# Kernel tuning notes

Measured on AMD Instinct MI355X. Metric: run time of the kernel, lower is better.

Reference implementation:

```python
import jax, jax.numpy as jnp
import numpy as np

D_MODEL = 1024
STATE_DIM = 256
BATCH = 4
SEQ_LEN = 4096


def setup_inputs() -> dict:
    key = jax.random.key(0)
    k_u, k_B, k_C = jax.random.split(key, 3)
    u = jax.random.normal(k_u, (BATCH, SEQ_LEN, D_MODEL), dtype=jnp.float32)
    # parameters (as in torch init)
    log_lambda = jnp.linspace(2.94, 4.6, STATE_DIM, dtype=jnp.float32)
    # nn.Linear weight shape is [out_features, in_features]
    B_w = jax.random.normal(k_B, (STATE_DIM, D_MODEL), dtype=jnp.float32) / np.sqrt(D_MODEL)
    C_w = jax.random.normal(k_C, (D_MODEL, STATE_DIM), dtype=jnp.float32) / np.sqrt(STATE_DIM)
    D = jnp.ones((D_MODEL,), dtype=jnp.float32)
    return {"u": u, "log_lambda": log_lambda, "B_w": B_w, "C_w": C_w, "D": D}


def reference(u, log_lambda, B_w, C_w, D):
    batch, seq_len, d = u.shape
    # Bu = B(u): [B, L, N]
    Bu = jnp.einsum("bld,nd->bln", u, B_w)
    lam = jax.nn.sigmoid(log_lambda)                     # [N]
    t = jnp.arange(seq_len, dtype=lam.dtype)
    kernel = lam[None, :] ** t[:, None]                  # [L, N]
    # next power of two >= 2*L (static)
    fft_len = 1
    while fft_len < 2 * seq_len:
        fft_len *= 2
    K_hat = jnp.fft.rfft(kernel, n=fft_len, axis=0)      # [F, N]
    Bu_hat = jnp.fft.rfft(Bu, n=fft_len, axis=1)         # [B, F, N]
    h_hat = K_hat[None, :, :] * Bu_hat
    h = jnp.fft.irfft(h_hat, n=fft_len, axis=1)[:, :seq_len, :]  # [B, L, N]
    y = jnp.einsum("bln,dn->bld", h, C_w) + D * u
    return y
```

## Files before the change

### kernel.cpp

```cpp
#include <hip/hip_runtime.h>
#include <hip/hip_bf16.h>

#define D_MODEL 1024
#define STATE_N 256
#define BATCH 4
#define SEQ_LEN 4096
#define M_TOTAL (BATCH * SEQ_LEN)
#define NCHUNK 128
#define CHUNK (SEQ_LEN / NCHUNK)

typedef __attribute__((ext_vector_type(8))) short bf16x8;
typedef __attribute__((ext_vector_type(4))) short s16x4;
typedef __attribute__((ext_vector_type(2))) short s16x2;
typedef __attribute__((ext_vector_type(4))) float f32x4;

static __device__ inline short f2bf(float f) {
    union { float f; unsigned u; } v; v.f = f;
    unsigned r = v.u + 0x7FFFu + ((v.u >> 16) & 1u);
    return (short)(r >> 16);
}
static __device__ inline float bf2f(short s) {
    union { unsigned u; float f; } v;
    v.u = ((unsigned)(unsigned short)s) << 16;
    return v.f;
}
static __device__ inline float sigmoidf(float x) { return 1.0f / (1.0f + expf(-x)); }

#define GLOAD_LDS16(gp, lp)                                                     \
    __builtin_amdgcn_global_load_lds(                                           \
        (const __attribute__((address_space(1))) void*)(gp),                    \
        (__attribute__((address_space(3))) void*)(lp), 16, 0, 0)

#define WAITVM0   asm volatile("s_waitcnt vmcnt(0)" ::: "memory")
#define WAITLGKM0 asm volatile("s_waitcnt lgkmcnt(0)" ::: "memory")
#define BARRIER() do { __builtin_amdgcn_s_barrier(); asm volatile("" ::: "memory"); } while (0)

__global__ void prep(const float* __restrict__ Bw, const float* __restrict__ Cw,
                     const float* __restrict__ ll,
                     short* __restrict__ Bwt, short* __restrict__ Cwt,
                     float* __restrict__ W) {
    const int bx = blockIdx.x, tid = threadIdx.x;
    if (bx >= 256) {
        const int i = bx - 256, n = tid;
        W[i * 256 + n] = powf(sigmoidf(ll[n]), (float)(31 - i));
        return;
    }
    const int g = bx * 256 + tid;
    const float* s; short* d;
    if (g < 32768) {
        const int col = g & 127, kc = (g >> 7) & 7, kt = (g >> 10) & 15, cb = g >> 14;
        s = Bw + (size_t)(cb * 128 + col) * D_MODEL + kt * 64 + kc * 8;
        d = Bwt + (size_t)g * 8;
    } else {
        const int h = g - 32768;
        const int col = h & 63, ksq = (h >> 6) & 7, tt = (h >> 9) & 3, cb = h >> 11;
        s = Cw + (size_t)(cb * 64 + col) * STATE_N + tt * 64 + ksq * 8;
        d = Cwt + (size_t)h * 8;
    }
    const f32x4 v0 = *(const f32x4*)s;
    const f32x4 v1 = *(const f32x4*)(s + 4);
    bf16x8 r;
    #pragma unroll
    for (int q = 0; q < 4; ++q) { r[q] = f2bf(v0[q]); r[4 + q] = f2bf(v1[q]); }
    *(bf16x8*)d = r;
}

__global__ __launch_bounds__(256, 2) void gemm1(const float* __restrict__ u,
                                                const short* __restrict__ Bwt,
                                                const float* __restrict__ W,
                                                short* __restrict__ Bu,
                                                float* __restrict__ ends) {
    __shared__ short Ash[2][64 * 64];
    const int tid = threadIdx.x;
    const int lane = tid & 63, wave = tid >> 6;
    const int lr = lane & 15, kq = lane >> 4;
    const int wr = wave >> 1, wc = wave & 1;
    const int wg = ((blockIdx.x & 7) << 6) + (blockIdx.x >> 3);
    const int cb = wg & 1, strip = wg >> 1;
    const int m0 = strip * 64, n0 = cb * 128;

    const int a_r = tid >> 4, a_k = (tid & 15) * 4;
    const float* au = u + (size_t)(m0 + a_r) * D_MODEL + a_k;
    const int a_ch = (tid & 15) >> 1, a_half = (tid & 1) * 4;
    const short* bg = Bwt + (size_t)cb * 16 * 8192;

    f32x4 acc[2][4] = {};
    f32x4 ar0[4], ar1[4], ar2[4];
    bf16x8 bfr[2][2][4];

    #define LOADA(SET, KT)                                                       \
        do { _Pragma("unroll")                                                   \
             for (int i = 0; i < 4; ++i)                                         \
                 SET[i] = *(const f32x4*)(au + (size_t)i * 16 * D_MODEL + (KT) * 64); } while (0)
    #define WRITEA(BUF, SET)                                                     \
        do { _Pragma("unroll")                                                   \
             for (int i = 0; i < 4; ++i) {                                       \
                 const int row = i * 16 + a_r;                                   \
                 s16x4 wv;                                                       \
                 _Pragma("unroll")                                               \
                 for (int e = 0; e < 4; ++e) wv[e] = f2bf(SET[i][e]);            \
                 *(s16x4*)&Ash[BUF][(row * 8 + (a_ch ^ (row & 7))) * 8 + a_half] = wv; \
             } } while (0)
    #define LOADB(BUF, KT)                                                       \
        do { _Pragma("unroll")                                                   \
             for (int ks = 0; ks < 2; ++ks)                                      \
                 _Pragma("unroll")                                               \
                 for (int j = 0; j < 4; ++j)                                     \
                     bfr[BUF][ks][j] = *(const bf16x8*)(bg + (size_t)(KT) * 8192 \
                         + ((ks * 4 + kq) * 128 + wc * 64 + j * 16 + lr) * 8); } while (0)

    LOADA(ar0, 0);
    WRITEA(0, ar0);
    LOADA(ar1, 1);
    LOADA(ar2, 2);
    LOADB(0, 0);
    WAITLGKM0;
    BARRIER();

    #pragma unroll
    for (int t = 0; t < 16; ++t) {
        if (t < 15) {
            if (((t + 1) % 3) == 0)      WRITEA((t + 1) & 1, ar0);
            else if (((t + 1) % 3) == 1) WRITEA((t + 1) & 1, ar1);
            else                         WRITEA((t + 1) & 1, ar2);
        }
        if (t + 3 <= 15) {
            if (((t + 3) % 3) == 0)      LOADA(ar0, t + 3);
            else if (((t + 3) % 3) == 1) LOADA(ar1, t + 3);
            else                         LOADA(ar2, t + 3);
        }
        bf16x8 af[2][2];
        #pragma unroll
        for (int ks = 0; ks < 2; ++ks)
            #pragma unroll
            for (int i = 0; i < 2; ++i) {
                const int row = wr * 32 + i * 16 + lr;
                af[ks][i] = *(const bf16x8*)&Ash[t & 1][(row * 8 + ((ks * 4 + kq) ^ (row & 7))) * 8];
            }
        if (t < 15) LOADB((t + 1) & 1, t + 1);
        #pragma unroll
        for (int ks = 0; ks < 2; ++ks)
            #pragma unroll
            for (int i = 0; i < 2; ++i)
                #pragma unroll
                for (int j = 0; j < 4; ++j)
                    acc[i][j] = __builtin_amdgcn_mfma_f32_16x16x32_bf16(bfr[t & 1][ks][j], af[ks][i], acc[i][j], 0, 0, 0);
        WAITLGKM0;
        BARRIER();
    }
    #undef LOADA
    #undef WRITEA
    #undef LOADB

    #pragma unroll
    for (int i = 0; i < 2; ++i) {
        const int m = m0 + wr * 32 + i * 16 + lr;
        #pragma unroll
        for (int j = 0; j < 4; ++j) {
            const int n = n0 + wc * 64 + j * 16 + kq * 4;
            s16x4 st;
            #pragma unroll
            for (int r = 0; r < 4; ++r) st[r] = f2bf(acc[i][j][r]);
            *(s16x4*)(Bu + (size_t)m * STATE_N + n) = st;
        }
    }

    float part[4][4];
    #pragma unroll
    for (int j = 0; j < 4; ++j) {
        const int nb = n0 + wc * 64 + j * 16 + kq * 4;
        const f32x4 w0 = *(const f32x4*)(W + (size_t)lr * 256 + nb);
        const f32x4 w1 = *(const f32x4*)(W + (size_t)(16 + lr) * 256 + nb);
        #pragma unroll
        for (int r = 0; r < 4; ++r)
            part[j][r] = w0[r] * acc[0][j][r] + w1[r] * acc[1][j][r];
    }
    #pragma unroll
    for (int m = 1; m <= 8; m <<= 1)
        #pragma unroll
        for (int j = 0; j < 4; ++j)
            #pragma unroll
            for (int r = 0; r < 4; ++r)
                part[j][r] += __shfl_xor(part[j][r], m, 64);
    if (lr == 0) {
        const int cg = strip * 2 + wr;
        #pragma unroll
        for (int j = 0; j < 4; ++j) {
            f32x4 e;
            #pragma unroll
            for (int r = 0; r < 4; ++r) e[r] = part[j][r];
            *(f32x4*)(ends + (size_t)cg * STATE_N + n0 + wc * 64 + j * 16 + kq * 4) = e;
        }
    }
}

__global__ __launch_bounds__(256, 4) void gemm2(const short* __restrict__ Bu,
                                                const short* __restrict__ Cwt,
                                                const float* __restrict__ ll,
                                                const float* __restrict__ carries,
                                                const float* __restrict__ u,
                                                const float* __restrict__ Dv,
                                                float* __restrict__ y) {
    __shared__ short Ash[4][64 * 64];
    const int tid = threadIdx.x;
    const int lane = tid & 63, wave = tid >> 6;
    const int lr = lane & 15, kq = lane >> 4;
    const int wr = wave >> 1, wc = wave & 1;
    const int wg = ((blockIdx.x & 7) << 9) + (blockIdx.x >> 3);
    const int cb = wg & 15, strip = wg >> 4;
    const int m0 = strip * 64, n0 = cb * 64;

    const int ch = tid >> 7;
    const int cp = tid & 127;
    const int st = cp >> 5;
    const int c0 = (2 * cp) & 63;
    const int scc = c0 >> 3, scw = c0 & 7;

    const float2 lraw = *(const float2*)(ll + 2 * cp);
    const float2 car2 = *(const float2*)(carries + (size_t)(strip * 2 + ch) * STATE_N + 2 * cp);

    const int aslot0 = wave * 128 + lane, aslot1 = aslot0 + 64;
    const int arow0 = aslot0 >> 3, arow1 = aslot1 >> 3;
    const int ac = lane & 7;
    const short* ag0 = Bu + (size_t)(m0 + arow0) * STATE_N + ((ac ^ (arow0 & 7)) << 3);
    const short* ag1 = Bu + (size_t)(m0 + arow1) * STATE_N + ((ac ^ (arow1 & 7)) << 3);
    const short* bg = Cwt + (size_t)cb * 4096 * 4;

    #pragma unroll
    for (int t = 0; t < 4; ++t) {
        GLOAD_LDS16(ag0 + t * 64, (char*)&Ash[t][0] + aslot0 * 16);
        GLOAD_LDS16(ag1 + t * 64, (char*)&Ash[t][0] + aslot1 * 16);
    }
    WAITVM0;
    BARRIER();

    bf16x8 bfr[2][2][2];
    #define LOADB2(BUF, T)                                                       \
        do { _Pragma("unroll")                                                   \
             for (int ks = 0; ks < 2; ++ks)                                      \
                 _Pragma("unroll")                                               \
                 for (int j = 0; j < 2; ++j)                                     \
                     bfr[BUF][ks][j] = *(const bf16x8*)(bg + (size_t)(T) * 4096  \
                         + (((ks << 2) | kq) * 64 + wc * 32 + j * 16 + lr) * 8); } while (0)

    LOADB2(0, 0);

    {
        const float lam0 = sigmoidf(lraw.x), lam1 = sigmoidf(lraw.y);
        s16x2 rv[32];
        #pragma unroll
        for (int i = 0; i < 32; ++i)
            rv[i] = *(const s16x2*)&Ash[st][(ch * 32 + i) * 64 + ((scc ^ (i & 7)) << 3) + scw];
        float h0 = car2.x, h1 = car2.y;
        #pragma unroll
        for (int i = 0; i < 32; ++i) {
            h0 = fmaf(lam0, h0, bf2f(rv[i][0]));
            h1 = fmaf(lam1, h1, bf2f(rv[i][1]));
            s16x2 o; o[0] = f2bf(h0); o[1] = f2bf(h1);
            rv[i] = o;
        }
        #pragma unroll
        for (int i = 0; i < 32; ++i)
            *(s16x2*)&Ash[st][(ch * 32 + i) * 64 + ((scc ^ (i & 7)) << 3) + scw] = rv[i];
    }
    WAITLGKM0;
    BARRIER();

    f32x4 acc[2][2] = {};
    #pragma unroll
    for (int t = 0; t < 4; ++t) {
        bf16x8 af[2][2];
        #pragma unroll
        for (int ks = 0; ks < 2; ++ks)
            #pragma unroll
            for (int i = 0; i < 2; ++i) {
                const int row = wr * 32 + i * 16 + lr;
                af[ks][i] = *(const bf16x8*)&Ash[t][row * 64 + ((((ks << 2) | kq) ^ (row & 7)) << 3)];
            }
        if (t < 3) LOADB2((t + 1) & 1, t + 1);
        #pragma unroll
        for (int ks = 0; ks < 2; ++ks)
            #pragma unroll
            for (int i = 0; i < 2; ++i)
                #pragma unroll
                for (int j = 0; j < 2; ++j)
                    acc[i][j] = __builtin_amdgcn_mfma_f32_16x16x32_bf16(bfr[t & 1][ks][j], af[ks][i], acc[i][j], 0, 0, 0);
    }
    #undef LOADB2

    #pragma unroll
    for (int i = 0; i < 2; ++i) {
        const int m = m0 + wr * 32 + i * 16 + lr;
        #pragma unroll
        for (int j = 0; j < 2; ++j) {
            const int n = n0 + wc * 32 + j * 16 + kq * 4;
            const size_t o = (size_t)m * D_MODEL + n;
            const f32x4 uv = *(const f32x4*)(u + o);
            const f32x4 dv = *(const f32x4*)(Dv + n);
            f32x4 rv;
            #pragma unroll
            for (int q = 0; q < 4; ++q) rv[q] = fmaf(dv[q], uv[q], acc[i][j][q]);
            *(f32x4*)(y + o) = rv;
        }
    }
}

__global__ void scan_carry(const float* __restrict__ ends,
                           const float* __restrict__ log_lambda,
                           float* __restrict__ carries) {
    const int n = threadIdx.x;
    const int b = blockIdx.x;
    const float lam = sigmoidf(log_lambda[n]);
    const float lamC = powf(lam, (float)CHUNK);
    float carry = 0.0f;
    #pragma unroll 16
    for (int c = 0; c < NCHUNK; ++c) {
        const size_t o = ((size_t)(b * NCHUNK + c)) * STATE_N + n;
        carries[o] = carry;
        carry = fmaf(lamC, carry, ends[o]);
    }
}

extern "C" void kernel_launch(void* const* d_in, const int* in_sizes, int n_in,
                              void* d_out, int out_size, void* d_ws, size_t ws_size,
                              hipStream_t stream) {
    const float* u  = (const float*)d_in[0];
    const float* ll = (const float*)d_in[1];
    const float* Bw = (const float*)d_in[2];
    const float* Cw = (const float*)d_in[3];
    const float* Dv = (const float*)d_in[4];
    float* y = (float*)d_out;

    char* ws = (char*)d_ws;
    size_t off = 0;
    short* Bwt = (short*)(ws + off); off += (size_t)STATE_N * D_MODEL * 2;
    short* Cwt = (short*)(ws + off); off += (size_t)D_MODEL * STATE_N * 2;
    float* W   = (float*)(ws + off); off += (size_t)32 * STATE_N * 4;
    short* Bu  = (short*)(ws + off); off += (size_t)M_TOTAL * STATE_N * 2;
    float* ends = (float*)(ws + off); off += (size_t)BATCH * NCHUNK * STATE_N * 4;
    float* carries = (float*)(ws + off);

    prep<<<288, 256, 0, stream>>>(Bw, Cw, ll, Bwt, Cwt, W);
    gemm1<<<512, 256, 0, stream>>>(u, Bwt, W, Bu, ends);
    scan_carry<<<BATCH, STATE_N, 0, stream>>>(ends, ll, carries);
    gemm2<<<4096, 256, 0, stream>>>(Bu, Cwt, ll, carries, u, Dv, y);
}
```

Before: 69.83 us.

## Load gemm1 A fragments directly from global into registers, drop LDS staging

```diff
diff --git a/kernel.cpp b/kernel.cpp
--- a/kernel.cpp
+++ b/kernel.cpp
@@ -18,6 +18,10 @@
     union { float f; unsigned u; } v; v.f = f;
     unsigned r = v.u + 0x7FFFu + ((v.u >> 16) & 1u);
     return (short)(r >> 16);
+}
+static __device__ inline short f2bf_hw(float f) {
+    __hip_bfloat16 h = __float2bfloat16(f);
+    return *reinterpret_cast<const short*>(&h);
 }
 static __device__ inline float bf2f(short s) {
     union { unsigned u; float f; } v;
@@ -70,7 +74,6 @@
                                                 const float* __restrict__ W,
                                                 short* __restrict__ Bu,
                                                 float* __restrict__ ends) {
-    __shared__ short Ash[2][64 * 64];
     const int tid = threadIdx.x;
     const int lane = tid & 63, wave = tid >> 6;
     const int lr = lane & 15, kq = lane >> 4;
@@ -79,27 +82,23 @@
     const int cb = wg & 1, strip = wg >> 1;
     const int m0 = strip * 64, n0 = cb * 128;
 
-    const int a_r = tid >> 4, a_k = (tid & 15) * 4;
-    const float* au = u + (size_t)(m0 + a_r) * D_MODEL + a_k;
-    const int a_ch = (tid & 15) >> 1, a_half = (tid & 1) * 4;
+    const float* ap[4];
+    #pragma unroll
+    for (int f = 0; f < 4; ++f) {
+        const int ks = f >> 1, i = f & 1;
+        ap[f] = u + (size_t)(m0 + wr * 32 + i * 16 + lr) * D_MODEL + (ks * 4 + kq) * 8;
+    }
     const short* bg = Bwt + (size_t)cb * 16 * 8192;
 
+    f32x4 araw[2][4][2];
+    bf16x8 bfr[2][2][4];
     f32x4 acc[2][4] = {};
-    f32x4 ar0[4], ar1[4], ar2[4];
-    bf16x8 bfr[2][2][4];
-
-    #define LOADA(SET, KT)                                                       \
+
+    #define LOADA(BUF, KT)                                                       \
         do { _Pragma("unroll")                                                   \
-             for (int i = 0; i < 4; ++i)                                         \
-                 SET[i] = *(const f32x4*)(au + (size_t)i * 16 * D_MODEL + (KT) * 64); } while (0)
-    #define WRITEA(BUF, SET)                                                     \
-        do { _Pragma("unroll")                                                   \
-             for (int i = 0; i < 4; ++i) {                                       \
-                 const int row = i * 16 + a_r;                                   \
-                 s16x4 wv;                                                       \
-                 _Pragma("unroll")                                               \
-                 for (int e = 0; e < 4; ++e) wv[e] = f2bf(SET[i][e]);            \
-                 *(s16x4*)&Ash[BUF][(row * 8 + (a_ch ^ (row & 7))) * 8 + a_half] = wv; \
+             for (int f = 0; f < 4; ++f) {                                       \
+                 araw[BUF][f][0] = *(const f32x4*)(ap[f] + (KT) * 64);           \
+                 araw[BUF][f][1] = *(const f32x4*)(ap[f] + (KT) * 64 + 4);       \
              } } while (0)
     #define LOADB(BUF, KT)                                                       \
         do { _Pragma("unroll")                                                   \
@@ -109,47 +108,30 @@
                      bfr[BUF][ks][j] = *(const bf16x8*)(bg + (size_t)(KT) * 8192 \
                          + ((ks * 4 + kq) * 128 + wc * 64 + j * 16 + lr) * 8); } while (0)
 
-    LOADA(ar0, 0);
-    WRITEA(0, ar0);
-    LOADA(ar1, 1);
-    LOADA(ar2, 2);
+    LOADA(0, 0);
     LOADB(0, 0);
-    WAITLGKM0;
-    BARRIER();
 
     #pragma unroll
     for (int t = 0; t < 16; ++t) {
-        if (t < 15) {
-            if (((t + 1) % 3) == 0)      WRITEA((t + 1) & 1, ar0);
-            else if (((t + 1) % 3) == 1) WRITEA((t + 1) & 1, ar1);
-            else                         WRITEA((t + 1) & 1, ar2);
-        }
-        if (t + 3 <= 15) {
-            if (((t + 3) % 3) == 0)      LOADA(ar0, t + 3);
-            else if (((t + 3) % 3) == 1) LOADA(ar1, t + 3);
-            else                         LOADA(ar2, t + 3);
-        }
-        bf16x8 af[2][2];
-        #pragma unroll
-        for (int ks = 0; ks < 2; ++ks)
-            #pragma unroll
-            for (int i = 0; i < 2; ++i) {
-                const int row = wr * 32 + i * 16 + lr;
-                af[ks][i] = *(const bf16x8*)&Ash[t & 1][(row * 8 + ((ks * 4 + kq) ^ (row & 7))) * 8];
+        const int cur = t & 1;
+        if (t < 15) { LOADA(cur ^ 1, t + 1); LOADB(cur ^ 1, t + 1); }
+        bf16x8 af[4];
+        #pragma unroll
+        for (int f = 0; f < 4; ++f)
+            #pragma unroll
+            for (int e = 0; e < 4; ++e) {
+                af[f][e]     = f2bf_hw(araw[cur][f][0][e]);
+                af[f][4 + e] = f2bf_hw(araw[cur][f][1][e]);
             }
-        if (t < 15) LOADB((t + 1) & 1, t + 1);
         #pragma unroll
         for (int ks = 0; ks < 2; ++ks)
             #pragma unroll
             for (int i = 0; i < 2; ++i)
                 #pragma unroll
                 for (int j = 0; j < 4; ++j)
-                    acc[i][j] = __builtin_amdgcn_mfma_f32_16x16x32_bf16(bfr[t & 1][ks][j], af[ks][i], acc[i][j], 0, 0, 0);
-        WAITLGKM0;
-        BARRIER();
+                    acc[i][j] = __builtin_amdgcn_mfma_f32_16x16x32_bf16(bfr[cur][ks][j], af[ks * 2 + i], acc[i][j], 0, 0, 0);
     }
     #undef LOADA
-    #undef WRITEA
     #undef LOADB
 
     #pragma unroll
@@ -160,7 +142,7 @@
             const int n = n0 + wc * 64 + j * 16 + kq * 4;
             s16x4 st;
             #pragma unroll
-            for (int r = 0; r < 4; ++r) st[r] = f2bf(acc[i][j][r]);
+            for (int r = 0; r < 4; ++r) st[r] = f2bf_hw(acc[i][j][r]);
             *(s16x4*)(Bu + (size_t)m * STATE_N + n) = st;
         }
     }
```

New measurement: 92.69 us. 32.7% more time.
